# Kernel tuning notes

Measured on AMD Instinct MI355X. Metric: run time of the kernel, lower is better.

Reference implementation:

```python
import jax, jax.numpy as jnp
import numpy as np

B, N, C, H = 2, 2048, 1024, 16
D = C // H  # head dim = 64
SCALE = 1.0 / np.sqrt(D)
BASE = 10000.0  # ntk_factor=1.0 => base unchanged


def setup_inputs() -> dict:
    key = jax.random.key(0)
    k1, k2, k3, k4 = jax.random.split(key, 4)
    x = jax.random.normal(k1, (B, N, C), dtype=jnp.float32)
    Wqkv = jax.random.normal(k2, (C, 3 * C), dtype=jnp.float32) * (1.0 / np.sqrt(C))
    Wout = jax.random.normal(k3, (C, C), dtype=jnp.float32) * (1.0 / np.sqrt(C))
    bout = jax.random.normal(k4, (C,), dtype=jnp.float32) * 0.01
    return {"x": x, "Wqkv": Wqkv, "Wout": Wout, "bout": bout}


def _rope_tables(n, d, dtype):
    inv_freq = 1.0 / (BASE ** (jnp.arange(0, d, 2, dtype=jnp.float32) / d))
    t = jnp.arange(n, dtype=jnp.float32)
    freqs = t[:, None] * inv_freq[None, :]            # [N, D/2]
    cos = jnp.cos(freqs)[None, :, None, :].astype(dtype)  # [1,N,1,D/2]
    sin = jnp.sin(freqs)[None, :, None, :].astype(dtype)
    return cos, sin


def _apply_rope(u, cos, sin):
    # u: [B,N,H,D]; strided-halves RoPE variant (cat, not interleave)
    u1, u2 = u[..., ::2], u[..., 1::2]
    return jnp.concatenate([u1 * cos - u2 * sin, u1 * sin + u2 * cos], axis=-1)


def reference(x, Wqkv, Wout, bout):
    b, n, c = x.shape
    qkv = (x @ Wqkv).reshape(b, n, 3, H, D)
    q, k, v = qkv[:, :, 0], qkv[:, :, 1], qkv[:, :, 2]  # [B,N,H,D]
    cos, sin = _rope_tables(n, D, x.dtype)
    q = _apply_rope(q, cos, sin)
    k = _apply_rope(k, cos, sin)
    scores = jnp.einsum("bqhd,bkhd->bhqk", q, k) * SCALE
    causal = jnp.triu(jnp.ones((n, n), dtype=bool), k=1)
    scores = jnp.where(causal, -jnp.inf, scores)
    attn = jax.nn.softmax(scores, axis=-1)
    out = jnp.einsum("bhqk,bkhd->bqhd", attn, v).reshape(b, n, c)
    return out @ Wout + bout
```

## Files before the change

### kernel.cpp

```cpp
#include <hip/hip_runtime.h>
#include <hip/hip_bf16.h>
#include <math.h>

#define B_ 2
#define N_ 2048
#define C_ 1024
#define H_ 16
#define D_ 64
#define M_ 4096
#define QKV_N 3072
#define SCALE_ 0.125f
#define FIXM 8.0f

typedef unsigned short u16;
typedef unsigned int u32;
using bf16x8   = __attribute__((ext_vector_type(8))) __bf16;
using ushortx8 = __attribute__((ext_vector_type(8))) unsigned short;
using floatx4  = __attribute__((ext_vector_type(4))) float;

__device__ __forceinline__ float bf2f(u16 u) {
    union { u32 i; float f; } v; v.i = ((u32)u) << 16; return v.f;
}
__device__ __forceinline__ u16 f2bf(float f) {
    union { float f; u32 i; } v; v.f = f;
    u32 r = (v.i + 0x7fff + ((v.i >> 16) & 1)) >> 16;
    return (u16)r;
}
__device__ __forceinline__ u32 pk2bf(float a, float b) {
    __hip_bfloat162 h = __float22bfloat162_rn(make_float2(a, b));
    union { __hip_bfloat162 h; u32 u; } c; c.h = h; return c.u;
}

__device__ __forceinline__ void gl2lds16(const void* g, void* l) {
    __builtin_amdgcn_global_load_lds(
        (const __attribute__((address_space(1))) unsigned int*)(unsigned long long)g,
        (__attribute__((address_space(3))) unsigned int*)(unsigned long long)l,
        16, 0, 0);
}

__constant__ unsigned char UQI[24] = {7,15,15,14,14,6,13,13,12,12,5,11,11,10,10,4,9,9,8,8,3,2,1,0};
__constant__ unsigned char UT0[24] = {0,0,16,0,15,0,0,14,0,13,0,0,12,0,11,0,0,10,0,9,0,0,0,0};
__constant__ unsigned char UNT[24] = {16,16,16,15,15,14,14,14,13,13,12,12,12,11,11,10,10,10,9,9,8,6,4,2};

__device__ __forceinline__ void do_convtrans(const float* W, u16* Wt, int K, int N,
                                             int nb, int kb, int tid) {
    int n = nb * 256 + tid;
    int k0 = kb * 128;
    #pragma unroll
    for (int kk = 0; kk < 128; kk += 8) {
        ushortx8 v;
        #pragma unroll
        for (int j = 0; j < 8; j++)
            v[j] = f2bf(W[(size_t)(k0 + kk + j) * N + n]);
        *(ushortx8*)(&Wt[(size_t)n * K + k0 + kk]) = v;
    }
}

__global__ __launch_bounds__(256) void prep_kernel(
    const float* __restrict__ x, const float* __restrict__ Wqkv,
    float* __restrict__ cosT, float* __restrict__ sinT,
    u16* __restrict__ xb, u16* __restrict__ Wqkvt)
{
    int bid = blockIdx.x, tid = threadIdx.x;
    if (bid < 2048) {
        int i = bid * 256 + tid;
        const float4* p = (const float4*)x + (size_t)i * 2;
        float4 a = p[0], b = p[1];
        ushortx8 v;
        v[0] = f2bf(a.x); v[1] = f2bf(a.y); v[2] = f2bf(a.z); v[3] = f2bf(a.w);
        v[4] = f2bf(b.x); v[5] = f2bf(b.y); v[6] = f2bf(b.z); v[7] = f2bf(b.w);
        *(ushortx8*)(xb + (size_t)i * 8) = v;
    } else if (bid < 2304) {
        int idx = (bid - 2048) * 256 + tid;
        int n = idx >> 5, i = idx & 31;
        double inv = pow(10000.0, -(double)i / 32.0);
        double f = (double)n * inv;
        cosT[idx] = (float)cos(f);
        sinT[idx] = (float)sin(f);
    } else {
        int u = bid - 2304;
        do_convtrans(Wqkv, Wqkvt, C_, QKV_N, u % 12, u / 12, tid);
    }
}

__global__ __launch_bounds__(256) void wout_trans(const float* __restrict__ Wout,
                                                  u16* __restrict__ Woutt) {
    do_convtrans(Wout, Woutt, C_, C_, blockIdx.x % 4, blockIdx.x / 4, threadIdx.x);
}

__global__ __launch_bounds__(256) void gemm128(
    const u16* __restrict__ A, const u16* __restrict__ Bt,
    void* __restrict__ Cm, const float* __restrict__ bias, int fp32out,
    int M, int N, int K)
{
    __shared__ u16 As[128 * 32];
    __shared__ u16 Bs[128 * 32];
    const int t = threadIdx.x;
    const int w = t >> 6, lane = t & 63;
    const int quad = lane >> 4, cc = lane & 15;
    const int m0 = blockIdx.y * 128, n0 = blockIdx.x * 128;
    const int wm = (w >> 1) * 64, wn = (w & 1) * 64;

    floatx4 acc[4][4];
    floatx4 zero = {0.f, 0.f, 0.f, 0.f};
    #pragma unroll
    for (int i = 0; i < 4; i++)
        #pragma unroll
        for (int j = 0; j < 4; j++) acc[i][j] = zero;

    const int srow = lane >> 2, skof = (lane & 3) * 8;

    for (int k0 = 0; k0 < K; k0 += 32) {
        __syncthreads();
        #pragma unroll
        for (int c = 0; c < 2; c++) {
            int chunk = w * 2 + c;
            int row = chunk * 16 + srow;
            gl2lds16(A  + (size_t)(m0 + row) * K + k0 + skof, (char*)As + chunk * 1024);
            gl2lds16(Bt + (size_t)(n0 + row) * K + k0 + skof, (char*)Bs + chunk * 1024);
        }
        __syncthreads();

        bf16x8 af[4], bf[4];
        #pragma unroll
        for (int i = 0; i < 4; i++)
            af[i] = *(const bf16x8*)(&As[(wm + i * 16 + cc) * 32 + quad * 8]);
        #pragma unroll
        for (int j = 0; j < 4; j++)
            bf[j] = *(const bf16x8*)(&Bs[(wn + j * 16 + cc) * 32 + quad * 8]);
        #pragma unroll
        for (int i = 0; i < 4; i++)
            #pragma unroll
            for (int j = 0; j < 4; j++)
                acc[i][j] = __builtin_amdgcn_mfma_f32_16x16x32_bf16(af[i], bf[j], acc[i][j], 0, 0, 0);
    }

    #pragma unroll
    for (int i = 0; i < 4; i++)
        #pragma unroll
        for (int j = 0; j < 4; j++)
            #pragma unroll
            for (int r = 0; r < 4; r++) {
                int row = m0 + wm + i * 16 + quad * 4 + r;
                int col = n0 + wn + j * 16 + cc;
                float v = acc[i][j][r];
                if (fp32out) ((float*)Cm)[(size_t)row * N + col] = v + bias[col];
                else         ((u16*)Cm)[(size_t)row * N + col] = f2bf(v);
            }
}

__global__ void rope_kernel(const u16* __restrict__ qkv,
                            const float* __restrict__ cosT, const float* __restrict__ sinT,
                            u16* __restrict__ Qh, u16* __restrict__ Kh, u16* __restrict__ Vh)
{
    int idx = blockIdx.x * 256 + threadIdx.x;
    if (idx >= B_ * N_ * H_ * 32) return;
    int i = idx & 31;
    int h = (idx >> 5) & (H_ - 1);
    int n = (idx >> 9) & (N_ - 1);
    int b = idx >> 20;
    size_t m = (size_t)b * N_ + n;
    const u16* row = qkv + m * QKV_N;
    float cs = cosT[n * 32 + i], sn = sinT[n * 32 + i];

    float q1 = bf2f(row[h * 64 + 2 * i]),      q2 = bf2f(row[h * 64 + 2 * i + 1]);
    float k1 = bf2f(row[C_ + h * 64 + 2 * i]), k2 = bf2f(row[C_ + h * 64 + 2 * i + 1]);
    size_t obase = ((size_t)(b * H_ + h) * N_ + n) * D_;
    Qh[obase + i]      = f2bf((q1 * cs - q2 * sn) * SCALE_);
    Qh[obase + 32 + i] = f2bf((q1 * sn + q2 * cs) * SCALE_);
    Kh[obase + i]      = f2bf(k1 * cs - k2 * sn);
    Kh[obase + 32 + i] = f2bf(k1 * sn + k2 * cs);
    Vh[obase + 2 * i]     = row[2 * C_ + h * 64 + 2 * i];
    Vh[obase + 2 * i + 1] = row[2 * C_ + h * 64 + 2 * i + 1];
}

__global__ __launch_bounds__(256) void attn_kernel(
    const u16* __restrict__ Qh, const u16* __restrict__ Kh,
    const u16* __restrict__ Vh, u16* __restrict__ Ao,
    float* __restrict__ Opart, float* __restrict__ lpart)
{
    constexpr int LDK = 66;
    __shared__ u16 Ks[2][64 * LDK];
    __shared__ u16 Vs[2][64 * LDK];
    __shared__ u16 Ps[4 * 32 * LDK];

    const int t = threadIdx.x;
    const int wave = t >> 6, lane = t & 63;
    const int quad = lane >> 4, cc = lane & 15;
    const int u = blockIdx.x;
    const int qi = UQI[u], tile0 = UT0[u], ntl = UNT[u];
    const int qb0 = qi * 128;
    const int bh = blockIdx.y;
    const size_t hb = (size_t)bh * N_ * D_;

    bf16x8 qf[2][2];
    #pragma unroll
    for (int qt = 0; qt < 2; qt++) {
        const u16* qrow = Qh + hb + (size_t)(qb0 + qt * 64 + wave * 16 + cc) * D_;
        qf[qt][0] = *(const bf16x8*)(qrow + quad * 8);
        qf[qt][1] = *(const bf16x8*)(qrow + 32 + quad * 8);
    }

    floatx4 zero = {0.f, 0.f, 0.f, 0.f};
    floatx4 Oacc[2][4];
    float lsum[2] = {0.f, 0.f};
    #pragma unroll
    for (int qt = 0; qt < 2; qt++)
        #pragma unroll
        for (int j = 0; j < 4; j++) Oacc[qt][j] = zero;

    const int krow = t >> 3, kch = (t & 7) * 8;
    const int kp = t >> 3, vchunk = (t & 7) * 8;
    const int qlocal = wave * 16 + cc;
    u32* psd = (u32*)Ps;

    bf16x8 kr[2]; ushortx8 vr[2];
    {
        int kb = tile0 * 64;
        kr[0] = *(const bf16x8*)(Kh + hb + (size_t)(kb + krow) * D_ + kch);
        kr[1] = *(const bf16x8*)(Kh + hb + (size_t)(kb + krow + 32) * D_ + kch);
        vr[0] = *(const ushortx8*)(Vh + hb + (size_t)(kb + 2 * kp) * D_ + vchunk);
        vr[1] = *(const ushortx8*)(Vh + hb + (size_t)(kb + 2 * kp + 1) * D_ + vchunk);
    }

    for (int ti = 0; ti < ntl; ti++) {
        const int kb = (tile0 + ti) * 64;
        const int c = ti & 1;
        *(bf16x8*)(&Ks[c][krow * LDK + kch]) = kr[0];
        *(bf16x8*)(&Ks[c][(krow + 32) * LDK + kch]) = kr[1];
        u32* vsd = (u32*)Vs[c];
        #pragma unroll
        for (int e = 0; e < 8; e++)
            vsd[(vchunk + e) * 33 + kp] = (u32)vr[0][e] | ((u32)vr[1][e] << 16);
        if (ti + 1 < ntl) {
            int kb2 = (tile0 + ti + 1) * 64;
            kr[0] = *(const bf16x8*)(Kh + hb + (size_t)(kb2 + krow) * D_ + kch);
            kr[1] = *(const bf16x8*)(Kh + hb + (size_t)(kb2 + krow + 32) * D_ + kch);
            vr[0] = *(const ushortx8*)(Vh + hb + (size_t)(kb2 + 2 * kp) * D_ + vchunk);
            vr[1] = *(const ushortx8*)(Vh + hb + (size_t)(kb2 + 2 * kp + 1) * D_ + vchunk);
        }
        __syncthreads();

        const bool act0 = (kb <= qb0);

        floatx4 S[2][4];
        #pragma unroll
        for (int nt = 0; nt < 4; nt++) {
            bf16x8 kf0 = *(const bf16x8*)(&Ks[c][(nt * 16 + cc) * LDK + quad * 8]);
            bf16x8 kf1 = *(const bf16x8*)(&Ks[c][(nt * 16 + cc) * LDK + 32 + quad * 8]);
            floatx4 a1 = zero;
            a1 = __builtin_amdgcn_mfma_f32_16x16x32_bf16(kf0, qf[1][0], a1, 0, 0, 0);
            a1 = __builtin_amdgcn_mfma_f32_16x16x32_bf16(kf1, qf[1][1], a1, 0, 0, 0);
            S[1][nt] = a1;
            if (act0) {
                floatx4 a0 = zero;
                a0 = __builtin_amdgcn_mfma_f32_16x16x32_bf16(kf0, qf[0][0], a0, 0, 0, 0);
                a0 = __builtin_amdgcn_mfma_f32_16x16x32_bf16(kf1, qf[0][1], a0, 0, 0, 0);
                S[0][nt] = a0;
            }
        }

        #pragma unroll
        for (int qt = 0; qt < 2; qt++) {
            if (qt == 0 && !act0) continue;
            const bool diag = (kb == qb0 + qt * 64);
            const int prow = (wave * 32 + qt * 16 + cc) * 33;
            #pragma unroll
            for (int nt = 0; nt < 4; nt++) {
                float p[4];
                #pragma unroll
                for (int r = 0; r < 4; r++) {
                    int key_l = nt * 16 + quad * 4 + r;
                    float e = __expf(S[qt][nt][r] - FIXM);
                    p[r] = (diag && (key_l > qlocal)) ? 0.0f : e;
                    lsum[qt] += p[r];
                }
                psd[prow + nt * 8 + quad * 2]     = pk2bf(p[0], p[1]);
                psd[prow + nt * 8 + quad * 2 + 1] = pk2bf(p[2], p[3]);
            }
        }

        #pragma unroll
        for (int s = 0; s < 2; s++) {
            bf16x8 pf1 = *(const bf16x8*)(&Ps[(wave * 32 + 16 + cc) * LDK + s * 32 + quad * 8]);
            bf16x8 pf0;
            if (act0) pf0 = *(const bf16x8*)(&Ps[(wave * 32 + cc) * LDK + s * 32 + quad * 8]);
            #pragma unroll
            for (int j = 0; j < 4; j++) {
                bf16x8 vf = *(const bf16x8*)(&Vs[c][(j * 16 + cc) * LDK + s * 32 + quad * 8]);
                Oacc[1][j] = __builtin_amdgcn_mfma_f32_16x16x32_bf16(pf1, vf, Oacc[1][j], 0, 0, 0);
                if (act0)
                    Oacc[0][j] = __builtin_amdgcn_mfma_f32_16x16x32_bf16(pf0, vf, Oacc[0][j], 0, 0, 0);
            }
        }
    }

    const bool partial = (qi >= 8);
    const int cid = (tile0 > 0) ? 1 : 0;
    const int slot = ((bh * 8 + (qi - 8)) * 2 + cid);
    const int b = bh >> 4, h = bh & (H_ - 1);

    #pragma unroll
    for (int qt = 0; qt < 2; qt++) {
        float lf = lsum[qt];
        lf += __shfl_xor(lf, 16, 64);
        lf += __shfl_xor(lf, 32, 64);
        if (!partial) {
            #pragma unroll
            for (int r = 0; r < 4; r++) {
                float l_r = __shfl(lf, quad * 4 + r, 64);
                float inv = 1.0f / l_r;
                int n = qb0 + qt * 64 + wave * 16 + quad * 4 + r;
                #pragma unroll
                for (int j = 0; j < 4; j++)
                    Ao[((size_t)b * N_ + n) * C_ + h * D_ + j * 16 + cc] = f2bf(Oacc[qt][j][r] * inv);
            }
        } else {
            #pragma unroll
            for (int r = 0; r < 4; r++) {
                int lrow = qt * 64 + wave * 16 + quad * 4 + r;
                float* Ob = Opart + (size_t)slot * (128 * 64) + (size_t)lrow * 64;
                #pragma unroll
                for (int j = 0; j < 4; j++)
                    Ob[j * 16 + cc] = Oacc[qt][j][r];
            }
            if (lane < 16)
                lpart[slot * 128 + qt * 64 + wave * 16 + cc] = lf;
        }
    }
}

__global__ __launch_bounds__(256) void attn_combine(
    const float* __restrict__ Opart, const float* __restrict__ lpart,
    u16* __restrict__ Ao)
{
    int g = blockIdx.x * 256 + threadIdx.x;
    int f4 = g & 15;
    int row = (g >> 4) & 127;
    int qz = (g >> 11) & 7;
    int bh = g >> 14;
    int s0 = (bh * 8 + qz) * 2;
    const float* O0 = Opart + (size_t)s0 * (128 * 64) + (size_t)row * 64 + f4 * 4;
    const float* O1 = O0 + 128 * 64;
    float l = lpart[s0 * 128 + row] + lpart[(s0 + 1) * 128 + row];
    float inv = 1.0f / l;
    float4 a = *(const float4*)O0, c = *(const float4*)O1;
    int b = bh >> 4, h = bh & (H_ - 1);
    int n = (qz + 8) * 128 + row;
    u16* d = Ao + ((size_t)b * N_ + n) * C_ + h * D_ + f4 * 4;
    d[0] = f2bf((a.x + c.x) * inv);
    d[1] = f2bf((a.y + c.y) * inv);
    d[2] = f2bf((a.z + c.z) * inv);
    d[3] = f2bf((a.w + c.w) * inv);
}

extern "C" void kernel_launch(void* const* d_in, const int* in_sizes, int n_in,
                              void* d_out, int out_size, void* d_ws, size_t ws_size,
                              hipStream_t stream)
{
    const float* x    = (const float*)d_in[0];
    const float* Wqkv = (const float*)d_in[1];
    const float* Wout = (const float*)d_in[2];
    const float* bout = (const float*)d_in[3];

    char* p = (char*)d_ws;
    u16* qkv = (u16*)p; p += (size_t)M_ * QKV_N * 2;
    u16* Qh  = (u16*)p; p += (size_t)B_ * H_ * N_ * D_ * 2;
    u16* Kh  = (u16*)p; p += (size_t)B_ * H_ * N_ * D_ * 2;
    u16* Vh  = (u16*)p; p += (size_t)B_ * H_ * N_ * D_ * 2;
    u16* Ao  = (u16*)p; p += (size_t)M_ * C_ * 2;
    float* cosT = (float*)p; p += (size_t)N_ * 32 * 4;
    float* sinT = (float*)p; p += (size_t)N_ * 32 * 4;

    u16* xb    = Ao;
    u16* Wqkvt = Qh;
    u16* Woutt = qkv;
    float* Opart = (float*)((char*)qkv + (2 << 20));
    float* lpart = (float*)((char*)qkv + (2 << 20) + 512 * 128 * 64 * 4);

    hipLaunchKernelGGL(prep_kernel, dim3(2400), dim3(256), 0, stream,
                       x, Wqkv, cosT, sinT, xb, Wqkvt);
    hipLaunchKernelGGL(gemm128, dim3(QKV_N / 128, M_ / 128), dim3(256), 0, stream,
                       xb, Wqkvt, qkv, (const float*)nullptr, 0, M_, QKV_N, C_);
    hipLaunchKernelGGL(rope_kernel, dim3((B_ * N_ * H_ * 32) / 256), dim3(256), 0, stream,
                       qkv, cosT, sinT, Qh, Kh, Vh);
    hipLaunchKernelGGL(wout_trans, dim3(32), dim3(256), 0, stream, Wout, Woutt);
    hipLaunchKernelGGL(attn_kernel, dim3(24, B_ * H_), dim3(256), 0, stream,
                       Qh, Kh, Vh, Ao, Opart, lpart);
    hipLaunchKernelGGL(attn_combine, dim3((32 * 8 * 128 * 16) / 256), dim3(256), 0, stream,
                       Opart, lpart, Ao);
    hipLaunchKernelGGL(gemm128, dim3(C_ / 128, M_ / 128), dim3(256), 0, stream,
                       Ao, Woutt, d_out, bout, 1, M_, C_, C_);
}
```

Before: 229.0 us.

## Fuse RoPE into QKV GEMM epilogue, rebalance causal attention split, bf16 partials

Fuses RoPE and the head-major scatter into the QKV GEMM epilogue, which drops the qkv round-trip and the separate rope kernel. It also folds the Wout transpose into the prep kernel. The attention work split grows from 24 to 40 units per head, with up to 4 chunks per query block, to balance causal work across blocks. Partial outputs are stored in bf16, combine sums a variable number of chunks, and exp becomes exp2 with a folded scale. The costs are scattered 2-byte stores in the GEMM epilogue, repeated cos/sin loads, and some precision loss in the partials.

```diff
diff --git a/kernel.cpp b/kernel.cpp
--- a/kernel.cpp
+++ b/kernel.cpp
@@ -11,6 +11,7 @@
 #define QKV_N 3072
 #define SCALE_ 0.125f
 #define FIXM 8.0f
+#define L2E 1.442695041f
 
 typedef unsigned short u16;
 typedef unsigned int u32;
@@ -38,9 +39,19 @@
         16, 0, 0);
 }
 
-__constant__ unsigned char UQI[24] = {7,15,15,14,14,6,13,13,12,12,5,11,11,10,10,4,9,9,8,8,3,2,1,0};
-__constant__ unsigned char UT0[24] = {0,0,16,0,15,0,0,14,0,13,0,0,12,0,11,0,0,10,0,9,0,0,0,0};
-__constant__ unsigned char UNT[24] = {16,16,16,15,15,14,14,14,13,13,12,12,12,11,11,10,10,10,9,9,8,6,4,2};
+__constant__ unsigned char UQI[40] = {15,15,15,15,14,14,11,11,11,10,7,7,3,
+                                      14,14,13,13,13,13,12,12,10,10,9,9,6,6,
+                                      12,12,9,8,8,8,5,5,2, 4,4,1,0};
+__constant__ unsigned char UT0[40] = {0,8,16,24,0,8,0,8,16,0,0,8,0,
+                                      16,23,0,7,14,21,0,7,8,15,0,7,0,7,
+                                      14,20,14,0,6,12,0,6,0, 0,5,0,0};
+__constant__ unsigned char UNT[40] = {8,8,8,8,8,8,8,8,8,8,8,8,8,
+                                      7,7,7,7,7,7,7,7,7,7,7,7,7,7,
+                                      6,6,6,6,6,6,6,6,6, 5,5,4,2};
+__constant__ unsigned char UCID[40] = {0,1,2,3,0,1,0,1,2,0,0,1,0,
+                                       2,3,0,1,2,3,0,1,1,2,0,1,0,1,
+                                       2,3,2,0,1,2,0,1,0, 0,1,0,0};
+__constant__ unsigned char SB[16] = {0,0,0,0, 0,2,4,6, 8,11,14,17, 20,24,28,32};
 
 __device__ __forceinline__ void do_convtrans(const float* W, u16* Wt, int K, int N,
                                              int nb, int kb, int tid) {
@@ -57,9 +68,9 @@
 }
 
 __global__ __launch_bounds__(256) void prep_kernel(
-    const float* __restrict__ x, const float* __restrict__ Wqkv,
+    const float* __restrict__ x, const float* __restrict__ Wqkv, const float* __restrict__ Wout,
     float* __restrict__ cosT, float* __restrict__ sinT,
-    u16* __restrict__ xb, u16* __restrict__ Wqkvt)
+    u16* __restrict__ xb, u16* __restrict__ Wqkvt, u16* __restrict__ Woutt)
 {
     int bid = blockIdx.x, tid = threadIdx.x;
     if (bid < 2048) {
@@ -77,21 +88,19 @@
         double f = (double)n * inv;
         cosT[idx] = (float)cos(f);
         sinT[idx] = (float)sin(f);
-    } else {
+    } else if (bid < 2400) {
         int u = bid - 2304;
         do_convtrans(Wqkv, Wqkvt, C_, QKV_N, u % 12, u / 12, tid);
-    }
-}
-
-__global__ __launch_bounds__(256) void wout_trans(const float* __restrict__ Wout,
-                                                  u16* __restrict__ Woutt) {
-    do_convtrans(Wout, Woutt, C_, C_, blockIdx.x % 4, blockIdx.x / 4, threadIdx.x);
-}
-
-__global__ __launch_bounds__(256) void gemm128(
+    } else {
+        int u = bid - 2400;
+        do_convtrans(Wout, Woutt, C_, C_, u % 4, u / 4, tid);
+    }
+}
+
+__global__ __launch_bounds__(256) void gemm_qkv_rope(
     const u16* __restrict__ A, const u16* __restrict__ Bt,
-    void* __restrict__ Cm, const float* __restrict__ bias, int fp32out,
-    int M, int N, int K)
+    const float* __restrict__ cosT, const float* __restrict__ sinT,
+    u16* __restrict__ Qh, u16* __restrict__ Kh, u16* __restrict__ Vh)
 {
     __shared__ u16 As[128 * 32];
     __shared__ u16 Bs[128 * 32];
@@ -100,6 +109,82 @@
     const int quad = lane >> 4, cc = lane & 15;
     const int m0 = blockIdx.y * 128, n0 = blockIdx.x * 128;
     const int wm = (w >> 1) * 64, wn = (w & 1) * 64;
+    const int K = C_;
+
+    floatx4 acc[4][4];
+    floatx4 zero = {0.f, 0.f, 0.f, 0.f};
+    #pragma unroll
+    for (int i = 0; i < 4; i++)
+        #pragma unroll
+        for (int j = 0; j < 4; j++) acc[i][j] = zero;
+
+    const int srow = lane >> 2, skof = (lane & 3) * 8;
+
+    for (int k0 = 0; k0 < K; k0 += 32) {
+        __syncthreads();
+        #pragma unroll
+        for (int c = 0; c < 2; c++) {
+            int chunk = w * 2 + c;
+            int row = chunk * 16 + srow;
+            gl2lds16(A  + (size_t)(m0 + row) * K + k0 + skof, (char*)As + chunk * 1024);
+            gl2lds16(Bt + (size_t)(n0 + row) * K + k0 + skof, (char*)Bs + chunk * 1024);
+        }
+        __syncthreads();
+
+        bf16x8 af[4], bf[4];
+        #pragma unroll
+        for (int i = 0; i < 4; i++)
+            af[i] = *(const bf16x8*)(&As[(wm + i * 16 + cc) * 32 + quad * 8]);
+        #pragma unroll
+        for (int j = 0; j < 4; j++)
+            bf[j] = *(const bf16x8*)(&Bs[(wn + j * 16 + cc) * 32 + quad * 8]);
+        #pragma unroll
+        for (int i = 0; i < 4; i++)
+            #pragma unroll
+            for (int j = 0; j < 4; j++)
+                acc[i][j] = __builtin_amdgcn_mfma_f32_16x16x32_bf16(af[i], bf[j], acc[i][j], 0, 0, 0);
+    }
+
+    const int sec = n0 >> 10;
+    #pragma unroll
+    for (int i = 0; i < 4; i++)
+        #pragma unroll
+        for (int j = 0; j < 4; j++) {
+            const int d = (wn + j * 16 + cc) & 63;
+            const int h = ((n0 & 1023) + wn + j * 16 + cc) >> 6;
+            const int ii = d >> 1;
+            #pragma unroll
+            for (int r = 0; r < 4; r++) {
+                int row = m0 + wm + i * 16 + quad * 4 + r;
+                int nseq = row & (N_ - 1), bb = row >> 11;
+                float v = acc[i][j][r];
+                size_t obase = (((size_t)(bb * H_ + h)) * N_ + nseq) * D_;
+                if (sec == 2) {
+                    Vh[obase + d] = f2bf(v);
+                } else {
+                    float pv = __shfl_xor(v, 1, 64);
+                    float cs = cosT[nseq * 32 + ii], sn = sinT[nseq * 32 + ii];
+                    float o = (d & 1) ? (pv * sn + v * cs) : (v * cs - pv * sn);
+                    int dd = (d & 1) ? (32 + ii) : ii;
+                    u16 res = f2bf(sec == 0 ? o * SCALE_ : o);
+                    (sec == 0 ? Qh : Kh)[obase + dd] = res;
+                }
+            }
+        }
+}
+
+__global__ __launch_bounds__(256) void gemm128(
+    const u16* __restrict__ A, const u16* __restrict__ Bt,
+    void* __restrict__ Cm, const float* __restrict__ bias, int fp32out,
+    int M, int N, int K)
+{
+    __shared__ u16 As[128 * 32];
+    __shared__ u16 Bs[128 * 32];
+    const int t = threadIdx.x;
+    const int w = t >> 6, lane = t & 63;
+    const int quad = lane >> 4, cc = lane & 15;
+    const int m0 = blockIdx.y * 128, n0 = blockIdx.x * 128;
+    const int wm = (w >> 1) * 64, wn = (w & 1) * 64;
 
     floatx4 acc[4][4];
     floatx4 zero = {0.f, 0.f, 0.f, 0.f};
@@ -149,35 +234,10 @@
             }
 }
 
-__global__ void rope_kernel(const u16* __restrict__ qkv,
-                            const float* __restrict__ cosT, const float* __restrict__ sinT,
-                            u16* __restrict__ Qh, u16* __restrict__ Kh, u16* __restrict__ Vh)
-{
-    int idx = blockIdx.x * 256 + threadIdx.x;
-    if (idx >= B_ * N_ * H_ * 32) return;
-    int i = idx & 31;
-    int h = (idx >> 5) & (H_ - 1);
-    int n = (idx >> 9) & (N_ - 1);
-    int b = idx >> 20;
-    size_t m = (size_t)b * N_ + n;
-    const u16* row = qkv + m * QKV_N;
-    float cs = cosT[n * 32 + i], sn = sinT[n * 32 + i];
-
-    float q1 = bf2f(row[h * 64 + 2 * i]),      q2 = bf2f(row[h * 64 + 2 * i + 1]);
-    float k1 = bf2f(row[C_ + h * 64 + 2 * i]), k2 = bf2f(row[C_ + h * 64 + 2 * i + 1]);
-    size_t obase = ((size_t)(b * H_ + h) * N_ + n) * D_;
-    Qh[obase + i]      = f2bf((q1 * cs - q2 * sn) * SCALE_);
-    Qh[obase + 32 + i] = f2bf((q1 * sn + q2 * cs) * SCALE_);
-    Kh[obase + i]      = f2bf(k1 * cs - k2 * sn);
-    Kh[obase + 32 + i] = f2bf(k1 * sn + k2 * cs);
-    Vh[obase + 2 * i]     = row[2 * C_ + h * 64 + 2 * i];
-    Vh[obase + 2 * i + 1] = row[2 * C_ + h * 64 + 2 * i + 1];
-}
-
 __global__ __launch_bounds__(256) void attn_kernel(
     const u16* __restrict__ Qh, const u16* __restrict__ Kh,
     const u16* __restrict__ Vh, u16* __restrict__ Ao,
-    float* __restrict__ Opart, float* __restrict__ lpart)
+    u16* __restrict__ Opart, float* __restrict__ lpart)
 {
     constexpr int LDK = 66;
     __shared__ u16 Ks[2][64 * LDK];
@@ -188,7 +248,7 @@
     const int wave = t >> 6, lane = t & 63;
     const int quad = lane >> 4, cc = lane & 15;
     const int u = blockIdx.x;
-    const int qi = UQI[u], tile0 = UT0[u], ntl = UNT[u];
+    const int qi = UQI[u], tile0 = UT0[u], ntl = UNT[u], cid = UCID[u];
     const int qb0 = qi * 128;
     const int bh = blockIdx.y;
     const size_t hb = (size_t)bh * N_ * D_;
@@ -271,7 +331,7 @@
                 #pragma unroll
                 for (int r = 0; r < 4; r++) {
                     int key_l = nt * 16 + quad * 4 + r;
-                    float e = __expf(S[qt][nt][r] - FIXM);
+                    float e = exp2f(fmaf(S[qt][nt][r], L2E, -FIXM * L2E));
                     p[r] = (diag && (key_l > qlocal)) ? 0.0f : e;
                     lsum[qt] += p[r];
                 }
@@ -295,9 +355,8 @@
         }
     }
 
-    const bool partial = (qi >= 8);
-    const int cid = (tile0 > 0) ? 1 : 0;
-    const int slot = ((bh * 8 + (qi - 8)) * 2 + cid);
+    const bool partial = (qi >= 4);
+    const int slot = bh * 36 + SB[qi] + cid;
     const int b = bh >> 4, h = bh & (H_ - 1);
 
     #pragma unroll
@@ -319,10 +378,10 @@
             #pragma unroll
             for (int r = 0; r < 4; r++) {
                 int lrow = qt * 64 + wave * 16 + quad * 4 + r;
-                float* Ob = Opart + (size_t)slot * (128 * 64) + (size_t)lrow * 64;
+                u16* Ob = Opart + (size_t)slot * (128 * 64) + (size_t)lrow * 64;
                 #pragma unroll
                 for (int j = 0; j < 4; j++)
-                    Ob[j * 16 + cc] = Oacc[qt][j][r];
+                    Ob[j * 16 + cc] = f2bf(Oacc[qt][j][r]);
             }
             if (lane < 16)
                 lpart[slot * 128 + qt * 64 + wave * 16 + cc] = lf;
@@ -331,27 +390,36 @@
 }
 
 __global__ __launch_bounds__(256) void attn_combine(
-    const float* __restrict__ Opart, const float* __restrict__ lpart,
+    const u16* __restrict__ Opart, const float* __restrict__ lpart,
     u16* __restrict__ Ao)
 {
     int g = blockIdx.x * 256 + threadIdx.x;
     int f4 = g & 15;
     int row = (g >> 4) & 127;
-    int qz = (g >> 11) & 7;
-    int bh = g >> 14;
-    int s0 = (bh * 8 + qz) * 2;
-    const float* O0 = Opart + (size_t)s0 * (128 * 64) + (size_t)row * 64 + f4 * 4;
-    const float* O1 = O0 + 128 * 64;
-    float l = lpart[s0 * 128 + row] + lpart[(s0 + 1) * 128 + row];
+    int rest = g >> 11;
+    int qq = rest % 12;
+    int bh = rest / 12;
+    int qi = qq + 4;
+    int nch = (qi >= 12) ? 4 : (qi >= 8) ? 3 : 2;
+    int s0 = bh * 36 + SB[qi];
+
+    float o[4] = {0.f, 0.f, 0.f, 0.f};
+    float l = 0.f;
+    for (int cch = 0; cch < nch; cch++) {
+        int slot = s0 + cch;
+        const u16* Ob = Opart + (size_t)slot * (128 * 64) + (size_t)row * 64 + f4 * 4;
+        ushort4 v = *(const ushort4*)Ob;
+        o[0] += bf2f(v.x); o[1] += bf2f(v.y); o[2] += bf2f(v.z); o[3] += bf2f(v.w);
+        l += lpart[slot * 128 + row];
+    }
     float inv = 1.0f / l;
-    float4 a = *(const float4*)O0, c = *(const float4*)O1;
     int b = bh >> 4, h = bh & (H_ - 1);
-    int n = (qz + 8) * 128 + row;
+    int n = qi * 128 + row;
     u16* d = Ao + ((size_t)b * N_ + n) * C_ + h * D_ + f4 * 4;
-    d[0] = f2bf((a.x + c.x) * inv);
-    d[1] = f2bf((a.y + c.y) * inv);
-    d[2] = f2bf((a.z + c.z) * inv);
-    d[3] = f2bf((a.w + c.w) * inv);
+    d[0] = f2bf(o[0] * inv);
+    d[1] = f2bf(o[1] * inv);
+    d[2] = f2bf(o[2] * inv);
+    d[3] = f2bf(o[3] * inv);
 }
 
 extern "C" void kernel_launch(void* const* d_in, const int* in_sizes, int n_in,
@@ -364,7 +432,7 @@
     const float* bout = (const float*)d_in[3];
 
     char* p = (char*)d_ws;
-    u16* qkv = (u16*)p; p += (size_t)M_ * QKV_N * 2;
+    char* reg1 = p;            p += (size_t)24 << 20;
     u16* Qh  = (u16*)p; p += (size_t)B_ * H_ * N_ * D_ * 2;
     u16* Kh  = (u16*)p; p += (size_t)B_ * H_ * N_ * D_ * 2;
     u16* Vh  = (u16*)p; p += (size_t)B_ * H_ * N_ * D_ * 2;
@@ -373,21 +441,18 @@
     float* sinT = (float*)p; p += (size_t)N_ * 32 * 4;
 
     u16* xb    = Ao;
-    u16* Wqkvt = Qh;
-    u16* Woutt = qkv;
-    float* Opart = (float*)((char*)qkv + (2 << 20));
-    float* lpart = (float*)((char*)qkv + (2 << 20) + 512 * 128 * 64 * 4);
-
-    hipLaunchKernelGGL(prep_kernel, dim3(2400), dim3(256), 0, stream,
-                       x, Wqkv, cosT, sinT, xb, Wqkvt);
-    hipLaunchKernelGGL(gemm128, dim3(QKV_N / 128, M_ / 128), dim3(256), 0, stream,
-                       xb, Wqkvt, qkv, (const float*)nullptr, 0, M_, QKV_N, C_);
-    hipLaunchKernelGGL(rope_kernel, dim3((B_ * N_ * H_ * 32) / 256), dim3(256), 0, stream,
-                       qkv, cosT, sinT, Qh, Kh, Vh);
-    hipLaunchKernelGGL(wout_trans, dim3(32), dim3(256), 0, stream, Wout, Woutt);
-    hipLaunchKernelGGL(attn_kernel, dim3(24, B_ * H_), dim3(256), 0, stream,
+    u16* Woutt = (u16*)reg1;
+    u16* Wqkvt = (u16*)(reg1 + ((size_t)2 << 20));
+    u16* Opart = (u16*)(reg1 + ((size_t)2 << 20));
+    float* lpart = (float*)(reg1 + ((size_t)21 << 20));
+
+    hipLaunchKernelGGL(prep_kernel, dim3(2432), dim3(256), 0, stream,
+                       x, Wqkv, Wout, cosT, sinT, xb, Wqkvt, Woutt);
+    hipLaunchKernelGGL(gemm_qkv_rope, dim3(QKV_N / 128, M_ / 128), dim3(256), 0, stream,
+                       xb, Wqkvt, cosT, sinT, Qh, Kh, Vh);
+    hipLaunchKernelGGL(attn_kernel, dim3(40, B_ * H_), dim3(256), 0, stream,
                        Qh, Kh, Vh, Ao, Opart, lpart);
-    hipLaunchKernelGGL(attn_combine, dim3((32 * 8 * 128 * 16) / 256), dim3(256), 0, stream,
+    hipLaunchKernelGGL(attn_combine, dim3((32 * 12 * 128 * 16) / 256), dim3(256), 0, stream,
                        Opart, lpart, Ao);
     hipLaunchKernelGGL(gemm128, dim3(C_ / 128, M_ / 128), dim3(256), 0, stream,
                        Ao, Woutt, d_out, bout, 1, M_, C_, C_);
```

Result: slower. 259.5 us (+13.3%).
